# Kernel tuning notes

Hardware: AMD Instinct MI355X
Metric: run time of the kernel (lower is better)

The kernel has to match this reference:

```python
import jax, jax.numpy as jnp
import numpy as np

B = 131072
D_IN = 128
D_H = 128


def _linear_params(key, fan_in, fan_out):
    # mimic nn.Linear init: U(-1/sqrt(fan_in), 1/sqrt(fan_in))
    kw, kb = jax.random.split(key)
    bound = 1.0 / np.sqrt(fan_in)
    W = jax.random.uniform(kw, (fan_in, fan_out), minval=-bound, maxval=bound, dtype=jnp.float32)
    b = jax.random.uniform(kb, (fan_out,), minval=-bound, maxval=bound, dtype=jnp.float32)
    return W, b


def setup_inputs() -> dict:
    key = jax.random.key(0)
    ks = jax.random.split(key, 12)
    inp = {
        'input': jax.random.normal(ks[0], (B, D_IN), dtype=jnp.float32),
        'seq_input': jax.random.normal(ks[1], (B, D_IN), dtype=jnp.float32),
        'hidden': jax.random.normal(ks[2], (B, D_H), dtype=jnp.float32),
    }
    names = ['ir', 'iz', 'in_', 'sr', 'sz', 'sn', 'hr', 'hz', 'hn']
    for i, nm in enumerate(names):
        fan_in = D_H if nm.startswith('h') else D_IN
        W, b = _linear_params(ks[3 + i], fan_in, D_H)
        inp['W_' + nm] = W
        inp['b_' + nm] = b
    return inp


def reference(input, seq_input, hidden,
              W_ir, b_ir, W_iz, b_iz, W_in_, b_in_,
              W_sr, b_sr, W_sz, b_sz, W_sn, b_sn,
              W_hr, b_hr, W_hz, b_hz, W_hn, b_hn):
    def lin(x, W, b):
        return x @ W + b

    hr = lin(hidden, W_hr, b_hr)  # shared between r_input and r_seq
    r_input = jax.nn.sigmoid(lin(input, W_ir, b_ir) + hr)
    r_seq = jax.nn.sigmoid(lin(seq_input, W_sr, b_sr) + hr)
    r = (r_input + r_seq) * 0.5

    hz = lin(hidden, W_hz, b_hz)
    z_input = jax.nn.sigmoid(lin(input, W_iz, b_iz) + hz)
    z_seq = jax.nn.sigmoid(lin(seq_input, W_sz, b_sz) + hz)
    z = (z_input + z_seq) * 0.5

    n = jnp.tanh(lin(input, W_in_, b_in_) + lin(seq_input, W_sn, b_sn)
                 + lin(r * hidden, W_hn, b_hn))
    new_hidden = (1.0 - z) * n + z * hidden
    return new_hidden
```

## Files before the change

kernel.cpp:

```cpp
#include <hip/hip_runtime.h>

#define BDIM 512
#define PACK_BDIM 256

typedef __attribute__((ext_vector_type(8))) short bf16x8;
typedef __attribute__((ext_vector_type(4))) float f32x4;
typedef __attribute__((ext_vector_type(4))) unsigned int u32x4;

__device__ __forceinline__ unsigned short f2b(float x) {
    unsigned u = __float_as_uint(x);
    return (unsigned short)((u + 0x7fffu + ((u >> 16) & 1u)) >> 16);
}
__device__ __forceinline__ float b2f(unsigned short b) {
    return __uint_as_float(((unsigned)b) << 16);
}

__global__ __launch_bounds__(PACK_BDIM) void pack_weights(
    const float* __restrict__ w0, const float* __restrict__ w1,
    const float* __restrict__ w2, const float* __restrict__ w3,
    const float* __restrict__ w4, const float* __restrict__ w5,
    const float* __restrict__ w6, const float* __restrict__ w7,
    const float* __restrict__ w8, unsigned short* __restrict__ wp)
{
    __shared__ float wsm[16384];
    const float* W;
    switch (blockIdx.x) {
        case 0: W = w0; break; case 1: W = w1; break; case 2: W = w2; break;
        case 3: W = w3; break; case 4: W = w4; break; case 5: W = w5; break;
        case 6: W = w6; break; case 7: W = w7; break; default: W = w8; break;
    }
    const int tid = threadIdx.x;
    for (int i = tid; i < 16384; i += PACK_BDIM) wsm[i] = W[i];
    __syncthreads();
    unsigned short* dst = wp + (size_t)blockIdx.x * 32768;
    for (int item = tid; item < 4096; item += PACK_BDIM) {
        const int lane = item & 63, q = item >> 6;
        const int s = q & 1, fc = q >> 1, f = fc & 7, c = fc >> 3;
        const int k0 = c * 32 + (lane >> 4) * 8;
        const int n  = f * 16 + (lane & 15);
        unsigned v2[4];
        for (int i2 = 0; i2 < 4; i2++) {
            unsigned short lohi[2];
            for (int t = 0; t < 2; t++) {
                float x = wsm[(k0 + i2 * 2 + t) * 128 + n];
                unsigned short hb = f2b(x);
                if (s) { hb = f2b(x - b2f(hb)); }
                lohi[t] = hb;
            }
            v2[i2] = (unsigned)lohi[0] | ((unsigned)lohi[1] << 16);
        }
        u32x4 vv; vv[0] = v2[0]; vv[1] = v2[1]; vv[2] = v2[2]; vv[3] = v2[3];
        *(u32x4*)(dst + (size_t)q * 512 + lane * 8) = vv;
    }
}

__global__ __launch_bounds__(BDIM) void gru_fused(
    const float* __restrict__ inp, const float* __restrict__ seqp,
    const float* __restrict__ hid, const unsigned short* __restrict__ wp,
    const float* __restrict__ b_ir, const float* __restrict__ b_iz,
    const float* __restrict__ b_in, const float* __restrict__ b_sr,
    const float* __restrict__ b_sz, const float* __restrict__ b_sn,
    const float* __restrict__ b_hr, const float* __restrict__ b_hz,
    const float* __restrict__ b_hn, float* __restrict__ outp)
{
    __shared__ unsigned short wbuf[32768];
    __shared__ float rbuf[16384];
    const int tid  = threadIdx.x;
    const int lane = tid & 63;
    const int wid  = tid >> 6;
    const int agrp = lane >> 4;
    const int a16  = lane & 15;
    const size_t row0 = (size_t)blockIdx.x * 128;

    const size_t arow = row0 + (size_t)(wid * 16 + a16);
    const float* pAin  = inp  + arow * 128;
    const float* pAseq = seqp + arow * 128;
    const float* pAhid = hid  + arow * 128;
    const int locrow_a = wid * 16 + a16;
    const int rsw = (locrow_a & 7) << 3;

    f32x4 hx[8], t[8], s1[8];
    const f32x4 zv = {0.f, 0.f, 0.f, 0.f};

    auto stage = [&](int g) {
        const u32x4* src = (const u32x4*)wp + (size_t)g * 4096;
        u32x4* dst = (u32x4*)wbuf;
        #pragma unroll
        for (int j = 0; j < 8; j++) dst[j * BDIM + tid] = src[j * BDIM + tid];
    };

    auto mm = [&](f32x4* acc, const float* pA, bool withR, bool init) {
        if (init) {
            #pragma unroll
            for (int f = 0; f < 8; f++) acc[f] = zv;
        }
        #pragma unroll
        for (int c = 0; c < 4; c++) {
            const float* p = pA + c * 32 + agrp * 8;
            f32x4 x0 = *(const f32x4*)(p);
            f32x4 x1 = *(const f32x4*)(p + 4);
            float xs[8];
            #pragma unroll
            for (int i = 0; i < 4; i++) { xs[i] = x0[i]; xs[4 + i] = x1[i]; }
            if (withR) {
                const int rk = (c * 32 + agrp * 8) ^ rsw;
                const f32x4 r0 = *(const f32x4*)(&rbuf[locrow_a * 128 + rk]);
                const f32x4 r1 = *(const f32x4*)(&rbuf[locrow_a * 128 + rk + 4]);
                #pragma unroll
                for (int i = 0; i < 4; i++) { xs[i] *= r0[i]; xs[4 + i] *= r1[i]; }
            }
            bf16x8 ah, al;
            #pragma unroll
            for (int i = 0; i < 8; i++) {
                float x = xs[i];
                unsigned short hb = f2b(x);
                ah[i] = (short)hb;
                al[i] = (short)f2b(x - b2f(hb));
            }
            #pragma unroll
            for (int f = 0; f < 8; f++) {
                const bf16x8 wh = *(const bf16x8*)(&wbuf[(size_t)((c * 8 + f) * 2 + 0) * 512 + lane * 8]);
                const bf16x8 wl = *(const bf16x8*)(&wbuf[(size_t)((c * 8 + f) * 2 + 1) * 512 + lane * 8]);
                acc[f] = __builtin_amdgcn_mfma_f32_16x16x32_bf16(ah, wh, acc[f], 0, 0, 0);
                acc[f] = __builtin_amdgcn_mfma_f32_16x16x32_bf16(al, wh, acc[f], 0, 0, 0);
                acc[f] = __builtin_amdgcn_mfma_f32_16x16x32_bf16(ah, wl, acc[f], 0, 0, 0);
            }
        }
    };

    auto addb = [&](f32x4* acc, const float* b) {
        #pragma unroll
        for (int f = 0; f < 8; f++) {
            float bv = b[f * 16 + a16];
            #pragma unroll
            for (int j = 0; j < 4; j++) acc[f][j] += bv;
        }
    };

    auto sigm = [](float x) { return 1.f / (1.f + __expf(-x)); };
    auto tanh_ = [](float x) {
        x = fminf(18.f, fmaxf(-18.f, x));
        float e = __expf(2.f * x);
        return (e - 1.f) / (e + 1.f);
    };

    stage(6); __syncthreads();
    mm(hx, pAhid, false, true); addb(hx, b_hr);
    __syncthreads(); stage(0); __syncthreads();
    mm(t, pAin, false, true);  addb(t, b_ir);
    #pragma unroll
    for (int f = 0; f < 8; f++)
        #pragma unroll
        for (int j = 0; j < 4; j++) s1[f][j] = sigm(t[f][j] + hx[f][j]);
    __syncthreads(); stage(3); __syncthreads();
    mm(t, pAseq, false, true); addb(t, b_sr);
    #pragma unroll
    for (int f = 0; f < 8; f++)
        #pragma unroll
        for (int j = 0; j < 4; j++) {
            float r = 0.5f * (s1[f][j] + sigm(t[f][j] + hx[f][j]));
            int row = wid * 16 + agrp * 4 + j;
            int col = f * 16 + a16;
            rbuf[row * 128 + (col ^ ((row & 7) << 3))] = r;
        }

    __syncthreads(); stage(7); __syncthreads();
    mm(hx, pAhid, false, true); addb(hx, b_hz);
    __syncthreads(); stage(1); __syncthreads();
    mm(t, pAin, false, true);  addb(t, b_iz);
    #pragma unroll
    for (int f = 0; f < 8; f++)
        #pragma unroll
        for (int j = 0; j < 4; j++) s1[f][j] = sigm(t[f][j] + hx[f][j]);
    __syncthreads(); stage(4); __syncthreads();
    mm(t, pAseq, false, true); addb(t, b_sz);
    #pragma unroll
    for (int f = 0; f < 8; f++)
        #pragma unroll
        for (int j = 0; j < 4; j++)
            s1[f][j] = 0.5f * (s1[f][j] + sigm(t[f][j] + hx[f][j]));

    __syncthreads(); stage(2); __syncthreads();
    mm(t, pAin, false, true);  addb(t, b_in);
    __syncthreads(); stage(5); __syncthreads();
    mm(t, pAseq, false, false); addb(t, b_sn);
    __syncthreads(); stage(8); __syncthreads();
    mm(t, pAhid, true, false); addb(t, b_hn);

    #pragma unroll
    for (int f = 0; f < 8; f++)
        #pragma unroll
        for (int j = 0; j < 4; j++) {
            int row = wid * 16 + agrp * 4 + j;
            size_t gidx = (row0 + row) * 128 + f * 16 + a16;
            float h  = hid[gidx];
            float nn = tanh_(t[f][j]);
            float zz = s1[f][j];
            outp[gidx] = (1.f - zz) * nn + zz * h;
        }
}

extern "C" void kernel_launch(void* const* d_in, const int* in_sizes, int n_in,
                              void* d_out, int out_size, void* d_ws, size_t ws_size,
                              hipStream_t stream)
{
    (void)in_sizes; (void)n_in; (void)out_size; (void)ws_size;
    const float* inp  = (const float*)d_in[0];
    const float* seqp = (const float*)d_in[1];
    const float* hid  = (const float*)d_in[2];
    const float* W[9]; const float* Bv[9];
    for (int i = 0; i < 9; i++) {
        W[i]  = (const float*)d_in[3 + 2 * i];
        Bv[i] = (const float*)d_in[4 + 2 * i];
    }
    unsigned short* wp = (unsigned short*)d_ws;

    pack_weights<<<9, PACK_BDIM, 0, stream>>>(W[0], W[1], W[2], W[3], W[4],
                                              W[5], W[6], W[7], W[8], wp);
    gru_fused<<<1024, BDIM, 0, stream>>>(inp, seqp, hid, wp,
                                         Bv[0], Bv[1], Bv[2], Bv[3], Bv[4],
                                         Bv[5], Bv[6], Bv[7], Bv[8],
                                         (float*)d_out);
}
```

Baseline: 323.1 us.

## Stage weights via direct global-to-LDS loads, drop rbuf, reorder gates to cut LDS

Weight staging now uses global_load_lds so tiles go straight from global memory into LDS without passing through registers. The separate r buffer is removed: the r gate is kept in registers and the weight buffer is reused as scratch. The n gate is computed before z, with tanh(n) spilled to the output and then blended in a coalesced vectorized pass. LDS per block is halved and launch bounds request higher occupancy, at the cost of an extra output round-trip and more syncs.

```diff
diff --git a/kernel.cpp b/kernel.cpp
--- a/kernel.cpp
+++ b/kernel.cpp
@@ -13,6 +13,12 @@
 }
 __device__ __forceinline__ float b2f(unsigned short b) {
     return __uint_as_float(((unsigned)b) << 16);
+}
+
+typedef __attribute__((address_space(1))) const unsigned int ga_u32;
+typedef __attribute__((address_space(3))) unsigned int la_u32;
+__device__ __forceinline__ void gload_lds16(const void* g, void* l) {
+    __builtin_amdgcn_global_load_lds((ga_u32*)g, (la_u32*)l, 16, 0, 0);
 }
 
 __global__ __launch_bounds__(PACK_BDIM) void pack_weights(
@@ -54,7 +60,7 @@
     }
 }
 
-__global__ __launch_bounds__(BDIM) void gru_fused(
+__global__ __launch_bounds__(BDIM, 4) void gru_fused(
     const float* __restrict__ inp, const float* __restrict__ seqp,
     const float* __restrict__ hid, const unsigned short* __restrict__ wp,
     const float* __restrict__ b_ir, const float* __restrict__ b_iz,
@@ -64,32 +70,36 @@
     const float* __restrict__ b_hn, float* __restrict__ outp)
 {
     __shared__ unsigned short wbuf[32768];
-    __shared__ float rbuf[16384];
+    float* tb = (float*)wbuf;
+
     const int tid  = threadIdx.x;
     const int lane = tid & 63;
     const int wid  = tid >> 6;
     const int agrp = lane >> 4;
     const int a16  = lane & 15;
     const size_t row0 = (size_t)blockIdx.x * 128;
-
-    const size_t arow = row0 + (size_t)(wid * 16 + a16);
-    const float* pAin  = inp  + arow * 128;
-    const float* pAseq = seqp + arow * 128;
-    const float* pAhid = hid  + arow * 128;
     const int locrow_a = wid * 16 + a16;
-    const int rsw = (locrow_a & 7) << 3;
-
-    f32x4 hx[8], t[8], s1[8];
+    const int rswA = (locrow_a & 7) << 3;
+
+    const float* pAin  = inp  + (row0 + locrow_a) * 128;
+    const float* pAseq = seqp + (row0 + locrow_a) * 128;
+    const float* pAhid = hid  + (row0 + locrow_a) * 128;
+
+    f32x4 hx[8], t[8], s1[8], rA[8];
     const f32x4 zv = {0.f, 0.f, 0.f, 0.f};
 
     auto stage = [&](int g) {
-        const u32x4* src = (const u32x4*)wp + (size_t)g * 4096;
-        u32x4* dst = (u32x4*)wbuf;
-        #pragma unroll
-        for (int j = 0; j < 8; j++) dst[j * BDIM + tid] = src[j * BDIM + tid];
-    };
-
-    auto mm = [&](f32x4* acc, const float* pA, bool withR, bool init) {
+        __syncthreads();
+        const char* src = (const char*)wp + (size_t)g * 65536;
+        #pragma unroll
+        for (int j = 0; j < 8; j++) {
+            const int off = (j * 8 + wid) * 1024;
+            gload_lds16(src + off + lane * 16, (char*)wbuf + off);
+        }
+        __syncthreads();
+    };
+
+    auto mm = [&](f32x4* acc, const float* pA, const f32x4* rAv, bool init) {
         if (init) {
             #pragma unroll
             for (int f = 0; f < 8; f++) acc[f] = zv;
@@ -99,23 +109,16 @@
             const float* p = pA + c * 32 + agrp * 8;
             f32x4 x0 = *(const f32x4*)(p);
             f32x4 x1 = *(const f32x4*)(p + 4);
-            float xs[8];
-            #pragma unroll
-            for (int i = 0; i < 4; i++) { xs[i] = x0[i]; xs[4 + i] = x1[i]; }
-            if (withR) {
-                const int rk = (c * 32 + agrp * 8) ^ rsw;
-                const f32x4 r0 = *(const f32x4*)(&rbuf[locrow_a * 128 + rk]);
-                const f32x4 r1 = *(const f32x4*)(&rbuf[locrow_a * 128 + rk + 4]);
-                #pragma unroll
-                for (int i = 0; i < 4; i++) { xs[i] *= r0[i]; xs[4 + i] *= r1[i]; }
-            }
+            if (rAv) { x0 *= rAv[2 * c]; x1 *= rAv[2 * c + 1]; }
             bf16x8 ah, al;
             #pragma unroll
-            for (int i = 0; i < 8; i++) {
-                float x = xs[i];
-                unsigned short hb = f2b(x);
+            for (int i = 0; i < 4; i++) {
+                unsigned short hb = f2b(x0[i]);
                 ah[i] = (short)hb;
-                al[i] = (short)f2b(x - b2f(hb));
+                al[i] = (short)(__float_as_uint(x0[i] - b2f(hb)) >> 16);
+                unsigned short hb1 = f2b(x1[i]);
+                ah[4 + i] = (short)hb1;
+                al[4 + i] = (short)(__float_as_uint(x1[i] - b2f(hb1)) >> 16);
             }
             #pragma unroll
             for (int f = 0; f < 8; f++) {
@@ -144,60 +147,92 @@
         return (e - 1.f) / (e + 1.f);
     };
 
-    stage(6); __syncthreads();
-    mm(hx, pAhid, false, true); addb(hx, b_hr);
-    __syncthreads(); stage(0); __syncthreads();
-    mm(t, pAin, false, true);  addb(t, b_ir);
+    stage(6);
+    mm(hx, pAhid, nullptr, true); addb(hx, b_hr);
+    stage(0);
+    mm(t, pAin, nullptr, true);  addb(t, b_ir);
     #pragma unroll
     for (int f = 0; f < 8; f++)
         #pragma unroll
         for (int j = 0; j < 4; j++) s1[f][j] = sigm(t[f][j] + hx[f][j]);
-    __syncthreads(); stage(3); __syncthreads();
-    mm(t, pAseq, false, true); addb(t, b_sr);
+    stage(3);
+    mm(t, pAseq, nullptr, true); addb(t, b_sr);
+    __syncthreads();
     #pragma unroll
     for (int f = 0; f < 8; f++)
         #pragma unroll
         for (int j = 0; j < 4; j++) {
-            float r = 0.5f * (s1[f][j] + sigm(t[f][j] + hx[f][j]));
             int row = wid * 16 + agrp * 4 + j;
             int col = f * 16 + a16;
-            rbuf[row * 128 + (col ^ ((row & 7) << 3))] = r;
-        }
-
-    __syncthreads(); stage(7); __syncthreads();
-    mm(hx, pAhid, false, true); addb(hx, b_hz);
-    __syncthreads(); stage(1); __syncthreads();
-    mm(t, pAin, false, true);  addb(t, b_iz);
-    #pragma unroll
-    for (int f = 0; f < 8; f++)
-        #pragma unroll
-        for (int j = 0; j < 4; j++) s1[f][j] = sigm(t[f][j] + hx[f][j]);
-    __syncthreads(); stage(4); __syncthreads();
-    mm(t, pAseq, false, true); addb(t, b_sz);
-    #pragma unroll
-    for (int f = 0; f < 8; f++)
-        #pragma unroll
-        for (int j = 0; j < 4; j++)
-            s1[f][j] = 0.5f * (s1[f][j] + sigm(t[f][j] + hx[f][j]));
-
-    __syncthreads(); stage(2); __syncthreads();
-    mm(t, pAin, false, true);  addb(t, b_in);
-    __syncthreads(); stage(5); __syncthreads();
-    mm(t, pAseq, false, false); addb(t, b_sn);
-    __syncthreads(); stage(8); __syncthreads();
-    mm(t, pAhid, true, false); addb(t, b_hn);
-
+            tb[row * 128 + (col ^ ((row & 7) << 3))] =
+                0.5f * (s1[f][j] + sigm(t[f][j] + hx[f][j]));
+        }
+    __syncthreads();
+    #pragma unroll
+    for (int c = 0; c < 4; c++) {
+        int rk = (c * 32 + agrp * 8) ^ rswA;
+        rA[2 * c]     = *(const f32x4*)(&tb[locrow_a * 128 + rk]);
+        rA[2 * c + 1] = *(const f32x4*)(&tb[locrow_a * 128 + rk + 4]);
+    }
+
+    stage(2);
+    mm(t, pAin, nullptr, true);  addb(t, b_in);
+    stage(5);
+    mm(t, pAseq, nullptr, false); addb(t, b_sn);
+    stage(8);
+    mm(t, pAhid, rA, false); addb(t, b_hn);
+    __syncthreads();
     #pragma unroll
     for (int f = 0; f < 8; f++)
         #pragma unroll
         for (int j = 0; j < 4; j++) {
             int row = wid * 16 + agrp * 4 + j;
-            size_t gidx = (row0 + row) * 128 + f * 16 + a16;
-            float h  = hid[gidx];
-            float nn = tanh_(t[f][j]);
-            float zz = s1[f][j];
-            outp[gidx] = (1.f - zz) * nn + zz * h;
-        }
+            int col = f * 16 + a16;
+            tb[row * 128 + (col ^ ((row & 7) << 3))] = tanh_(t[f][j]);
+        }
+    __syncthreads();
+    #pragma unroll
+    for (int p = 0; p < 8; p++) {
+        int e = p * 2048 + tid * 4;
+        int rrow = e >> 7, c0 = e & 127;
+        f32x4 v = *(const f32x4*)(&tb[rrow * 128 + (c0 ^ ((rrow & 7) << 3))]);
+        *(f32x4*)(&outp[(row0 + rrow) * 128 + c0]) = v;
+    }
+
+    stage(7);
+    mm(hx, pAhid, nullptr, true); addb(hx, b_hz);
+    stage(1);
+    mm(t, pAin, nullptr, true);  addb(t, b_iz);
+    #pragma unroll
+    for (int f = 0; f < 8; f++)
+        #pragma unroll
+        for (int j = 0; j < 4; j++) s1[f][j] = sigm(t[f][j] + hx[f][j]);
+    stage(4);
+    mm(t, pAseq, nullptr, true); addb(t, b_sz);
+    __syncthreads();
+    #pragma unroll
+    for (int f = 0; f < 8; f++)
+        #pragma unroll
+        for (int j = 0; j < 4; j++) {
+            int row = wid * 16 + agrp * 4 + j;
+            int col = f * 16 + a16;
+            tb[row * 128 + (col ^ ((row & 7) << 3))] =
+                0.5f * (s1[f][j] + sigm(t[f][j] + hx[f][j]));
+        }
+    __syncthreads();
+    #pragma unroll
+    for (int p = 0; p < 8; p++) {
+        int e = p * 2048 + tid * 4;
+        int rrow = e >> 7, c0 = e & 127;
+        size_t gbase = (row0 + rrow) * 128 + c0;
+        f32x4 z = *(const f32x4*)(&tb[rrow * 128 + (c0 ^ ((rrow & 7) << 3))]);
+        f32x4 nv = *(const f32x4*)(&outp[gbase]);
+        f32x4 h  = *(const f32x4*)(&hid[gbase]);
+        f32x4 o;
+        #pragma unroll
+        for (int j = 0; j < 4; j++) o[j] = (1.f - z[j]) * nv[j] + z[j] * h[j];
+        *(f32x4*)(&outp[gbase]) = o;
+    }
 }
 
 extern "C" void kernel_launch(void* const* d_in, const int* in_sizes, int n_in,
```

New measurement: 358.3 us. +10.9%, slower.
